# Kernel optimization log

Hardware: AMD Instinct MI355X
Metric: run time of the kernel (lower is better)

The kernel has to match this reference:

```python
import jax, jax.numpy as jnp
import numpy as np

D_MODEL = 1024
D_STATE = 16
DT_RANK = 64  # ceil(1024/16)
DT_MIN, DT_MAX = 1e-3, 1e-1


def setup_inputs() -> dict:
    key = jax.random.key(0)
    ks = jax.random.split(key, 6)
    x = jax.random.normal(ks[0], (2, 2048, D_MODEL), jnp.float32)
    A_log = jax.random.normal(ks[1], (D_MODEL, D_STATE), jnp.float32)
    D = jax.random.normal(ks[2], (D_MODEL,), jnp.float32)
    # nn.Linear default init ~ U(-1/sqrt(fan_in), 1/sqrt(fan_in)); normal*scale is fine for a baseline
    x_proj_w = jax.random.normal(ks[3], (DT_RANK + 2 * D_STATE, D_MODEL), jnp.float32) * (D_MODEL ** -0.5)
    dt_init_std = DT_RANK ** -0.5
    dt_proj_w = jax.random.uniform(ks[4], (D_MODEL, DT_RANK), jnp.float32, -dt_init_std, dt_init_std)
    dt = jnp.exp(jax.random.uniform(ks[5], (D_MODEL,), jnp.float32)
                 * (np.log(DT_MAX) - np.log(DT_MIN)) + np.log(DT_MIN))
    dt_proj_b = dt + jnp.log(-jnp.expm1(-dt))  # inverse-softplus init
    return {"x": x, "A_log": A_log, "D": D, "x_proj_w": x_proj_w,
            "dt_proj_w": dt_proj_w, "dt_proj_b": dt_proj_b}


def _s6(x, A_log, D, x_proj_w, dt_proj_w, dt_proj_b):
    A = -jnp.exp(A_log)                                    # (d, n)
    xp = jnp.einsum('bld,ed->ble', x, x_proj_w)            # (b, l, r+2n)
    d_rank = xp[..., :DT_RANK]
    Bm = xp[..., DT_RANK:DT_RANK + D_STATE]                # (b, l, n)
    Cm = xp[..., DT_RANK + D_STATE:]                       # (b, l, n)
    delta = jax.nn.softplus(jnp.einsum('blr,dr->bld', d_rank, dt_proj_w) + dt_proj_b)
    deltaA = jnp.exp(jnp.einsum('bld,dn->bldn', delta, A))          # (b, l, d, n)
    deltaB_u = jnp.einsum('bld,bln,bld->bldn', delta, Bm, x)        # (b, l, d, n)

    def step(h, inp):
        dA_t, dBu_t, C_t = inp          # (b,d,n), (b,d,n), (b,n)
        h = dA_t * h + dBu_t
        y = jnp.einsum('bdn,bn->bd', h, C_t)
        return h, y

    b, l, d = x.shape
    h0 = jnp.zeros((b, d, D_STATE), x.dtype)
    _, ys = jax.lax.scan(step, h0,
                         (deltaA.transpose(1, 0, 2, 3),
                          deltaB_u.transpose(1, 0, 2, 3),
                          Cm.transpose(1, 0, 2)))
    y = ys.transpose(1, 0, 2) + x * D                      # (b, l, d)
    return y


def reference(x, A_log, D, x_proj_w, dt_proj_w, dt_proj_b):
    return _s6(x, A_log, D, x_proj_w, dt_proj_w, dt_proj_b)
```

## Files before the change

### kernel.cpp

```cpp
#include <hip/hip_runtime.h>
#include <math.h>

#define Bb 2
#define Ll 2048
#define Dm 1024
#define Ns 16
#define Rr 64
#define Ee 96
#define XPS 8
#define BLK (Bb*Ll)
#define NTHR 256

__global__ void __launch_bounds__(NTHR)
k_xproj(const float* __restrict__ x, const float* __restrict__ xw,
        float* __restrict__ xp_part) {
    __shared__ float xsT[32 * 68];
    __shared__ float wT [32 * 100];
    int bx = blockIdx.x;
    int ks = bx & 7, mt = bx >> 3;
    int i0 = mt * 64;
    int tid = threadIdx.x;
    int tx = tid & 15, ty = tid >> 4;

    float acc[4][6];
#pragma unroll
    for (int ii = 0; ii < 4; ++ii)
#pragma unroll
        for (int jj = 0; jj < 6; ++jj) acc[ii][jj] = 0.f;

    for (int kc = 0; kc < 4; ++kc) {
        int k0 = ks * 128 + kc * 32;
        for (int t = tid; t < 512; t += NTHR) {
            int r = t >> 3, c = (t & 7) * 4;
            float4 v = *(const float4*)(x + (size_t)(i0 + r) * Dm + k0 + c);
            xsT[(c+0)*68 + r] = v.x; xsT[(c+1)*68 + r] = v.y;
            xsT[(c+2)*68 + r] = v.z; xsT[(c+3)*68 + r] = v.w;
        }
        for (int t = tid; t < 768; t += NTHR) {
            int r = t >> 3, c = (t & 7) * 4;
            float4 v = *(const float4*)(xw + (size_t)r * Dm + k0 + c);
            wT[(c+0)*100 + r] = v.x; wT[(c+1)*100 + r] = v.y;
            wT[(c+2)*100 + r] = v.z; wT[(c+3)*100 + r] = v.w;
        }
        __syncthreads();
#pragma unroll 8
        for (int k = 0; k < 32; ++k) {
            float xv[4], wv[6];
            *(float4*)xv     = *(const float4*)(xsT + k*68 + ty*4);
            *(float2*)(wv)   = *(const float2*)(wT + k*100 + tx*6);
            *(float2*)(wv+2) = *(const float2*)(wT + k*100 + tx*6 + 2);
            *(float2*)(wv+4) = *(const float2*)(wT + k*100 + tx*6 + 4);
#pragma unroll
            for (int ii = 0; ii < 4; ++ii)
#pragma unroll
                for (int jj = 0; jj < 6; ++jj)
                    acc[ii][jj] = fmaf(xv[ii], wv[jj], acc[ii][jj]);
        }
        __syncthreads();
    }
#pragma unroll
    for (int ii = 0; ii < 4; ++ii)
#pragma unroll
        for (int jj = 0; jj < 6; ++jj)
            xp_part[((size_t)ks * BLK + (i0 + ty*4 + ii)) * Ee + tx*6 + jj] = acc[ii][jj];
}

__global__ void __launch_bounds__(NTHR)
k_prep(const float* __restrict__ xp_part, float* __restrict__ xpR,
       float* __restrict__ xpBC) {
    int gid = blockIdx.x * NTHR + threadIdx.x;
    int r = gid / 24, c4 = gid % 24;
    float4 s = make_float4(0.f, 0.f, 0.f, 0.f);
#pragma unroll
    for (int i = 0; i < XPS; ++i) {
        float4 v = *(const float4*)(xp_part + ((size_t)i * BLK + r) * Ee + c4 * 4);
        s.x += v.x; s.y += v.y; s.z += v.z; s.w += v.w;
    }
    if (c4 < 16) *(float4*)(xpR  + (size_t)r * Rr + c4 * 4)        = s;
    else         *(float4*)(xpBC + (size_t)r * 32 + (c4 - 16) * 4) = s;
}

__global__ void __launch_bounds__(NTHR)
k_delta(const float* __restrict__ xpR, const float* __restrict__ dtw,
        const float* __restrict__ dtb, float* __restrict__ delta) {
    __shared__ float xsT[64 * 68];
    __shared__ float wT [64 * 68];
    int bx = blockIdx.x;
    int nt = bx & 15, mt = bx >> 4;
    int i0 = mt * 64, j0 = nt * 64;
    int tid = threadIdx.x, tx = tid & 15, ty = tid >> 4;

    for (int t = tid; t < 1024; t += NTHR) {
        int r = t >> 4, c = (t & 15) * 4;
        float4 v = *(const float4*)(xpR + (size_t)(i0 + r) * Rr + c);
        xsT[(c+0)*68 + r] = v.x; xsT[(c+1)*68 + r] = v.y;
        xsT[(c+2)*68 + r] = v.z; xsT[(c+3)*68 + r] = v.w;
        float4 w = *(const float4*)(dtw + (size_t)(j0 + r) * Rr + c);
        wT[(c+0)*68 + r] = w.x; wT[(c+1)*68 + r] = w.y;
        wT[(c+2)*68 + r] = w.z; wT[(c+3)*68 + r] = w.w;
    }
    __syncthreads();

    float acc[4][4];
#pragma unroll
    for (int ii = 0; ii < 4; ++ii)
#pragma unroll
        for (int jj = 0; jj < 4; ++jj) acc[ii][jj] = 0.f;
#pragma unroll 8
    for (int k = 0; k < 64; ++k) {
        float xv[4], wv[4];
        *(float4*)xv = *(const float4*)(xsT + k*68 + ty*4);
        *(float4*)wv = *(const float4*)(wT  + k*68 + tx*4);
#pragma unroll
        for (int ii = 0; ii < 4; ++ii)
#pragma unroll
            for (int jj = 0; jj < 4; ++jj)
                acc[ii][jj] = fmaf(xv[ii], wv[jj], acc[ii][jj]);
    }
    int d0 = j0 + tx * 4;
    float4 bias = *(const float4*)(dtb + d0);
#pragma unroll
    for (int ii = 0; ii < 4; ++ii) {
        int bl = i0 + ty*4 + ii;
        float z0 = acc[ii][0] + bias.x, z1 = acc[ii][1] + bias.y;
        float z2 = acc[ii][2] + bias.z, z3 = acc[ii][3] + bias.w;
        float4 o;
        o.x = fmaxf(z0, 0.f) + log1pf(__expf(-fabsf(z0)));
        o.y = fmaxf(z1, 0.f) + log1pf(__expf(-fabsf(z1)));
        o.z = fmaxf(z2, 0.f) + log1pf(__expf(-fabsf(z2)));
        o.w = fmaxf(z3, 0.f) + log1pf(__expf(-fabsf(z3)));
        *(float4*)(delta + (size_t)bl * Dm + d0) = o;
    }
}

__device__ inline void load_a(const float* __restrict__ A_log, int d, float* a) {
    const float4* Ap = (const float4*)(A_log + (size_t)d * Ns);
    float4 a0 = Ap[0], a1 = Ap[1], a2 = Ap[2], a3 = Ap[3];
    float tmp[Ns] = {a0.x,a0.y,a0.z,a0.w, a1.x,a1.y,a1.z,a1.w,
                     a2.x,a2.y,a2.z,a2.w, a3.x,a3.y,a3.z,a3.w};
#pragma unroll
    for (int n = 0; n < Ns; ++n) a[n] = -__expf(tmp[n]);
}

template<int CHv>
__global__ void __launch_bounds__(NTHR, 4)
k_scan_part(const float* __restrict__ delta, const float* __restrict__ x,
            const float* __restrict__ xpBC, const float* __restrict__ A_log,
            float* __restrict__ Ec, float* __restrict__ Sc) {
    constexpr int CLv = Ll / CHv;
    __shared__ float BCs[CLv * 32];
    int bx = blockIdx.x;
    int dblk = bx & 3, chunk = (bx >> 2) & (CHv - 1), b = bx >> 2 >> __builtin_ctz(CHv);
    int tid = threadIdx.x;
    int d = dblk * 256 + tid;
    int row0 = b * Ll + chunk * CLv;

    for (int t = tid; t < CLv * 8; t += NTHR) {
        int r = t >> 3, c = (t & 7) * 4;
        *(float4*)(BCs + r*32 + c) = *(const float4*)(xpBC + (size_t)(row0 + r) * 32 + c);
    }
    float a[Ns], h[Ns];
    load_a(A_log, d, a);
#pragma unroll
    for (int n = 0; n < Ns; ++n) h[n] = 0.f;
    float sd = 0.f;
    __syncthreads();

#pragma unroll 4
    for (int t = 0; t < CLv; ++t) {
        size_t row = (size_t)(row0 + t);
        float dl = delta[row * Dm + d];
        float xv = x[row * Dm + d];
        const float* bp = BCs + t*32;
        float4 B0 = *(const float4*)(bp + 0),  B1 = *(const float4*)(bp + 4);
        float4 B2 = *(const float4*)(bp + 8),  B3 = *(const float4*)(bp + 12);
        float Bv[Ns] = {B0.x,B0.y,B0.z,B0.w, B1.x,B1.y,B1.z,B1.w,
                        B2.x,B2.y,B2.z,B2.w, B3.x,B3.y,B3.z,B3.w};
        float dx = dl * xv;
        sd += dl;
#pragma unroll
        for (int n = 0; n < Ns; ++n)
            h[n] = fmaf(__expf(dl * a[n]), h[n], dx * Bv[n]);
    }
    size_t base = ((size_t)b * CHv + chunk) * Dm + d;
    float4* Ep = (float4*)(Ec + base * Ns);
    Ep[0] = make_float4(h[0],  h[1],  h[2],  h[3]);
    Ep[1] = make_float4(h[4],  h[5],  h[6],  h[7]);
    Ep[2] = make_float4(h[8],  h[9],  h[10], h[11]);
    Ep[3] = make_float4(h[12], h[13], h[14], h[15]);
    Sc[base] = sd;
}

template<int CHv>
__global__ void __launch_bounds__(NTHR)
k_combine(const float* __restrict__ Ec, const float* __restrict__ Sc,
          const float* __restrict__ A_log, float* __restrict__ Hin) {
    int gid = blockIdx.x * NTHR + threadIdx.x;
    int n = gid & (Ns - 1);
    int d = (gid >> 4) & (Dm - 1);
    int b = gid >> 14;
    float a = -__expf(A_log[d * Ns + n]);
    float h = 0.f;
    for (int c = 0; c < CHv; ++c) {
        size_t base = ((size_t)b * CHv + c) * Dm + d;
        Hin[base * Ns + n] = h;
        float P = __expf(a * Sc[base]);
        h = fmaf(P, h, Ec[base * Ns + n]);
    }
}

template<int CHv>
__global__ void __launch_bounds__(NTHR, 4)
k_scan_full(const float* __restrict__ delta, const float* __restrict__ x,
            const float* __restrict__ xpBC, const float* __restrict__ A_log,
            const float* __restrict__ Dp, const float* __restrict__ Hin,
            float* __restrict__ out) {
    constexpr int CLv = Ll / CHv;
    __shared__ float BCs[CLv * 32];
    int bx = blockIdx.x;
    int dblk = bx & 3, chunk = (bx >> 2) & (CHv - 1), b = bx >> 2 >> __builtin_ctz(CHv);
    int tid = threadIdx.x;
    int d = dblk * 256 + tid;
    int row0 = b * Ll + chunk * CLv;

    for (int t = tid; t < CLv * 8; t += NTHR) {
        int r = t >> 3, c = (t & 7) * 4;
        *(float4*)(BCs + r*32 + c) = *(const float4*)(xpBC + (size_t)(row0 + r) * 32 + c);
    }
    float a[Ns], h[Ns];
    load_a(A_log, d, a);
    size_t base = ((size_t)b * CHv + chunk) * Dm + d;
    {
        const float4* Hp = (const float4*)(Hin + base * Ns);
        float4 h0 = Hp[0], h1 = Hp[1], h2 = Hp[2], h3 = Hp[3];
        h[0]=h0.x; h[1]=h0.y; h[2]=h0.z; h[3]=h0.w;
        h[4]=h1.x; h[5]=h1.y; h[6]=h1.z; h[7]=h1.w;
        h[8]=h2.x; h[9]=h2.y; h[10]=h2.z; h[11]=h2.w;
        h[12]=h3.x; h[13]=h3.y; h[14]=h3.z; h[15]=h3.w;
    }
    float Dval = Dp[d];
    __syncthreads();

#pragma unroll 4
    for (int t = 0; t < CLv; ++t) {
        size_t row = (size_t)(row0 + t);
        float dl = delta[row * Dm + d];
        float xv = x[row * Dm + d];
        const float* bp = BCs + t*32;
        float4 B0 = *(const float4*)(bp + 0),  B1 = *(const float4*)(bp + 4);
        float4 B2 = *(const float4*)(bp + 8),  B3 = *(const float4*)(bp + 12);
        float4 C0 = *(const float4*)(bp + 16), C1 = *(const float4*)(bp + 20);
        float4 C2 = *(const float4*)(bp + 24), C3 = *(const float4*)(bp + 28);
        float Bv[Ns] = {B0.x,B0.y,B0.z,B0.w, B1.x,B1.y,B1.z,B1.w,
                        B2.x,B2.y,B2.z,B2.w, B3.x,B3.y,B3.z,B3.w};
        float Cv[Ns] = {C0.x,C0.y,C0.z,C0.w, C1.x,C1.y,C1.z,C1.w,
                        C2.x,C2.y,C2.z,C2.w, C3.x,C3.y,C3.z,C3.w};
        float dx = dl * xv;
        float y = 0.f;
#pragma unroll
        for (int n = 0; n < Ns; ++n) {
            h[n] = fmaf(__expf(dl * a[n]), h[n], dx * Bv[n]);
            y = fmaf(h[n], Cv[n], y);
        }
        out[row * Dm + d] = fmaf(xv, Dval, y);
    }
}

extern "C" void kernel_launch(void* const* d_in, const int* in_sizes, int n_in,
                              void* d_out, int out_size, void* d_ws, size_t ws_size,
                              hipStream_t stream) {
    const float* x     = (const float*)d_in[0];
    const float* A_log = (const float*)d_in[1];
    const float* Dp    = (const float*)d_in[2];
    const float* xw    = (const float*)d_in[3];
    const float* dtw   = (const float*)d_in[4];
    const float* dtb   = (const float*)d_in[5];
    float* out = (float*)d_out;
    float* ws  = (float*)d_ws;

    float* xpR     = ws;
    float* xpBC    = xpR  + 262144;
    float* delta   = xpBC + 131072;
    float* S3      = delta + 4194304;
    float* xp_part = S3;

    k_xproj<<<dim3(512),  dim3(NTHR), 0, stream>>>(x, xw, xp_part);
    k_prep <<<dim3(384),  dim3(NTHR), 0, stream>>>(xp_part, xpR, xpBC);
    k_delta<<<dim3(1024), dim3(NTHR), 0, stream>>>(xpR, dtw, dtb, delta);

    size_t need128 = (size_t)(262144 + 131072 + 4194304 + 8650752) * 4;
    if (ws_size >= need128) {
        constexpr int CHv = 128;
        float* Ec  = S3;
        float* Sc  = Ec + (size_t)Bb*CHv*Dm*Ns;
        float* Hin = Sc + (size_t)Bb*CHv*Dm;
        k_scan_part<CHv><<<dim3(Bb*CHv*4), dim3(NTHR), 0, stream>>>(delta, x, xpBC, A_log, Ec, Sc);
        k_combine  <CHv><<<dim3(128),      dim3(NTHR), 0, stream>>>(Ec, Sc, A_log, Hin);
        k_scan_full<CHv><<<dim3(Bb*CHv*4), dim3(NTHR), 0, stream>>>(delta, x, xpBC, A_log, Dp, Hin, out);
    } else {
        constexpr int CHv = 64;
        float* Ec  = S3;
        float* Sc  = Ec + (size_t)Bb*CHv*Dm*Ns;
        float* Hin = Sc + (size_t)Bb*CHv*Dm;
        k_scan_part<CHv><<<dim3(Bb*CHv*4), dim3(NTHR), 0, stream>>>(delta, x, xpBC, A_log, Ec, Sc);
        k_combine  <CHv><<<dim3(128),      dim3(NTHR), 0, stream>>>(Ec, Sc, A_log, Hin);
        k_scan_full<CHv><<<dim3(Bb*CHv*4), dim3(NTHR), 0, stream>>>(delta, x, xpBC, A_log, Dp, Hin, out);
    }
}
```

Baseline: 167.5 us.

## Fuse split-K reduction into delta GEMM and fix scan chunk count at 64

Removes the k_prep kernel: the delta GEMM now sums the split-K partials of the x-projection while loading its tile, and blocks with nt==0 also write the B/C columns. Scan kernels drop the workspace-size branch and template and always use 64 chunks of 32 steps, with a simplified shared-memory load and no occupancy hint. This saves a launch and an intermediate buffer round trip. In exchange, every delta block re-reads eight partial slices, and each scan thread runs a longer serial chain across fewer blocks.

Measured after the change: 179.1 us. 1.07x slower.

```diff
diff --git a/kernel.cpp b/kernel.cpp
--- a/kernel.cpp
+++ b/kernel.cpp
@@ -10,6 +10,8 @@
 #define XPS 8
 #define BLK (Bb*Ll)
 #define NTHR 256
+#define CH 64
+#define CL 32
 
 __global__ void __launch_bounds__(NTHR)
 k_xproj(const float* __restrict__ x, const float* __restrict__ xw,
@@ -66,23 +68,9 @@
 }
 
 __global__ void __launch_bounds__(NTHR)
-k_prep(const float* __restrict__ xp_part, float* __restrict__ xpR,
-       float* __restrict__ xpBC) {
-    int gid = blockIdx.x * NTHR + threadIdx.x;
-    int r = gid / 24, c4 = gid % 24;
-    float4 s = make_float4(0.f, 0.f, 0.f, 0.f);
-#pragma unroll
-    for (int i = 0; i < XPS; ++i) {
-        float4 v = *(const float4*)(xp_part + ((size_t)i * BLK + r) * Ee + c4 * 4);
-        s.x += v.x; s.y += v.y; s.z += v.z; s.w += v.w;
-    }
-    if (c4 < 16) *(float4*)(xpR  + (size_t)r * Rr + c4 * 4)        = s;
-    else         *(float4*)(xpBC + (size_t)r * 32 + (c4 - 16) * 4) = s;
-}
-
-__global__ void __launch_bounds__(NTHR)
-k_delta(const float* __restrict__ xpR, const float* __restrict__ dtw,
-        const float* __restrict__ dtb, float* __restrict__ delta) {
+k_delta(const float* __restrict__ xp_part, const float* __restrict__ dtw,
+        const float* __restrict__ dtb, float* __restrict__ delta,
+        float* __restrict__ xpBC) {
     __shared__ float xsT[64 * 68];
     __shared__ float wT [64 * 68];
     int bx = blockIdx.x;
@@ -92,12 +80,29 @@
 
     for (int t = tid; t < 1024; t += NTHR) {
         int r = t >> 4, c = (t & 15) * 4;
-        float4 v = *(const float4*)(xpR + (size_t)(i0 + r) * Rr + c);
-        xsT[(c+0)*68 + r] = v.x; xsT[(c+1)*68 + r] = v.y;
-        xsT[(c+2)*68 + r] = v.z; xsT[(c+3)*68 + r] = v.w;
+        float4 s = make_float4(0.f, 0.f, 0.f, 0.f);
+#pragma unroll
+        for (int i = 0; i < XPS; ++i) {
+            float4 v = *(const float4*)(xp_part + ((size_t)i * BLK + i0 + r) * Ee + c);
+            s.x += v.x; s.y += v.y; s.z += v.z; s.w += v.w;
+        }
+        xsT[(c+0)*68 + r] = s.x; xsT[(c+1)*68 + r] = s.y;
+        xsT[(c+2)*68 + r] = s.z; xsT[(c+3)*68 + r] = s.w;
         float4 w = *(const float4*)(dtw + (size_t)(j0 + r) * Rr + c);
         wT[(c+0)*68 + r] = w.x; wT[(c+1)*68 + r] = w.y;
         wT[(c+2)*68 + r] = w.z; wT[(c+3)*68 + r] = w.w;
+    }
+    if (nt == 0) {
+        for (int t = tid; t < 512; t += NTHR) {
+            int r = t >> 3, cc = (t & 7) * 4;
+            float4 s = make_float4(0.f, 0.f, 0.f, 0.f);
+#pragma unroll
+            for (int i = 0; i < XPS; ++i) {
+                float4 v = *(const float4*)(xp_part + ((size_t)i * BLK + i0 + r) * Ee + Rr + cc);
+                s.x += v.x; s.y += v.y; s.z += v.z; s.w += v.w;
+            }
+            *(float4*)(xpBC + (size_t)(i0 + r) * 32 + cc) = s;
+        }
     }
     __syncthreads();
 
@@ -142,21 +147,19 @@
     for (int n = 0; n < Ns; ++n) a[n] = -__expf(tmp[n]);
 }
 
-template<int CHv>
-__global__ void __launch_bounds__(NTHR, 4)
+__global__ void __launch_bounds__(NTHR)
 k_scan_part(const float* __restrict__ delta, const float* __restrict__ x,
             const float* __restrict__ xpBC, const float* __restrict__ A_log,
             float* __restrict__ Ec, float* __restrict__ Sc) {
-    constexpr int CLv = Ll / CHv;
-    __shared__ float BCs[CLv * 32];
-    int bx = blockIdx.x;
-    int dblk = bx & 3, chunk = (bx >> 2) & (CHv - 1), b = bx >> 2 >> __builtin_ctz(CHv);
+    __shared__ float BCs[CL * 32];
+    int bx = blockIdx.x;
+    int dblk = bx & 3, chunk = (bx >> 2) & (CH - 1), b = bx >> 8;
     int tid = threadIdx.x;
     int d = dblk * 256 + tid;
-    int row0 = b * Ll + chunk * CLv;
-
-    for (int t = tid; t < CLv * 8; t += NTHR) {
-        int r = t >> 3, c = (t & 7) * 4;
+    int row0 = b * Ll + chunk * CL;
+
+    {
+        int r = tid >> 3, c = (tid & 7) * 4;
         *(float4*)(BCs + r*32 + c) = *(const float4*)(xpBC + (size_t)(row0 + r) * 32 + c);
     }
     float a[Ns], h[Ns];
@@ -167,7 +170,7 @@
     __syncthreads();
 
 #pragma unroll 4
-    for (int t = 0; t < CLv; ++t) {
+    for (int t = 0; t < CL; ++t) {
         size_t row = (size_t)(row0 + t);
         float dl = delta[row * Dm + d];
         float xv = x[row * Dm + d];
@@ -182,7 +185,7 @@
         for (int n = 0; n < Ns; ++n)
             h[n] = fmaf(__expf(dl * a[n]), h[n], dx * Bv[n]);
     }
-    size_t base = ((size_t)b * CHv + chunk) * Dm + d;
+    size_t base = ((size_t)b * CH + chunk) * Dm + d;
     float4* Ep = (float4*)(Ec + base * Ns);
     Ep[0] = make_float4(h[0],  h[1],  h[2],  h[3]);
     Ep[1] = make_float4(h[4],  h[5],  h[6],  h[7]);
@@ -191,7 +194,6 @@
     Sc[base] = sd;
 }
 
-template<int CHv>
 __global__ void __launch_bounds__(NTHR)
 k_combine(const float* __restrict__ Ec, const float* __restrict__ Sc,
           const float* __restrict__ A_log, float* __restrict__ Hin) {
@@ -201,35 +203,34 @@
     int b = gid >> 14;
     float a = -__expf(A_log[d * Ns + n]);
     float h = 0.f;
-    for (int c = 0; c < CHv; ++c) {
-        size_t base = ((size_t)b * CHv + c) * Dm + d;
+#pragma unroll 4
+    for (int c = 0; c < CH; ++c) {
+        size_t base = ((size_t)b * CH + c) * Dm + d;
         Hin[base * Ns + n] = h;
         float P = __expf(a * Sc[base]);
         h = fmaf(P, h, Ec[base * Ns + n]);
     }
 }
 
-template<int CHv>
-__global__ void __launch_bounds__(NTHR, 4)
+__global__ void __launch_bounds__(NTHR)
 k_scan_full(const float* __restrict__ delta, const float* __restrict__ x,
             const float* __restrict__ xpBC, const float* __restrict__ A_log,
             const float* __restrict__ Dp, const float* __restrict__ Hin,
             float* __restrict__ out) {
-    constexpr int CLv = Ll / CHv;
-    __shared__ float BCs[CLv * 32];
-    int bx = blockIdx.x;
-    int dblk = bx & 3, chunk = (bx >> 2) & (CHv - 1), b = bx >> 2 >> __builtin_ctz(CHv);
+    __shared__ float BCs[CL * 32];
+    int bx = blockIdx.x;
+    int dblk = bx & 3, chunk = (bx >> 2) & (CH - 1), b = bx >> 8;
     int tid = threadIdx.x;
     int d = dblk * 256 + tid;
-    int row0 = b * Ll + chunk * CLv;
-
-    for (int t = tid; t < CLv * 8; t += NTHR) {
-        int r = t >> 3, c = (t & 7) * 4;
+    int row0 = b * Ll + chunk * CL;
+
+    {
+        int r = tid >> 3, c = (tid & 7) * 4;
         *(float4*)(BCs + r*32 + c) = *(const float4*)(xpBC + (size_t)(row0 + r) * 32 + c);
     }
     float a[Ns], h[Ns];
     load_a(A_log, d, a);
-    size_t base = ((size_t)b * CHv + chunk) * Dm + d;
+    size_t base = ((size_t)b * CH + chunk) * Dm + d;
     {
         const float4* Hp = (const float4*)(Hin + base * Ns);
         float4 h0 = Hp[0], h1 = Hp[1], h2 = Hp[2], h3 = Hp[3];
@@ -242,7 +243,7 @@
     __syncthreads();
 
 #pragma unroll 4
-    for (int t = 0; t < CLv; ++t) {
+    for (int t = 0; t < CL; ++t) {
         size_t row = (size_t)(row0 + t);
         float dl = delta[row * Dm + d];
         float xv = x[row * Dm + d];
@@ -278,32 +279,16 @@
     float* out = (float*)d_out;
     float* ws  = (float*)d_ws;
 
-    float* xpR     = ws;
-    float* xpBC    = xpR  + 262144;
-    float* delta   = xpBC + 131072;
-    float* S3      = delta + 4194304;
-    float* xp_part = S3;
-
-    k_xproj<<<dim3(512),  dim3(NTHR), 0, stream>>>(x, xw, xp_part);
-    k_prep <<<dim3(384),  dim3(NTHR), 0, stream>>>(xp_part, xpR, xpBC);
-    k_delta<<<dim3(1024), dim3(NTHR), 0, stream>>>(xpR, dtw, dtb, delta);
-
-    size_t need128 = (size_t)(262144 + 131072 + 4194304 + 8650752) * 4;
-    if (ws_size >= need128) {
-        constexpr int CHv = 128;
-        float* Ec  = S3;
-        float* Sc  = Ec + (size_t)Bb*CHv*Dm*Ns;
-        float* Hin = Sc + (size_t)Bb*CHv*Dm;
-        k_scan_part<CHv><<<dim3(Bb*CHv*4), dim3(NTHR), 0, stream>>>(delta, x, xpBC, A_log, Ec, Sc);
-        k_combine  <CHv><<<dim3(128),      dim3(NTHR), 0, stream>>>(Ec, Sc, A_log, Hin);
-        k_scan_full<CHv><<<dim3(Bb*CHv*4), dim3(NTHR), 0, stream>>>(delta, x, xpBC, A_log, Dp, Hin, out);
-    } else {
-        constexpr int CHv = 64;
-        float* Ec  = S3;
-        float* Sc  = Ec + (size_t)Bb*CHv*Dm*Ns;
-        float* Hin = Sc + (size_t)Bb*CHv*Dm;
-        k_scan_part<CHv><<<dim3(Bb*CHv*4), dim3(NTHR), 0, stream>>>(delta, x, xpBC, A_log, Ec, Sc);
-        k_combine  <CHv><<<dim3(128),      dim3(NTHR), 0, stream>>>(Ec, Sc, A_log, Hin);
-        k_scan_full<CHv><<<dim3(Bb*CHv*4), dim3(NTHR), 0, stream>>>(delta, x, xpBC, A_log, Dp, Hin, out);
-    }
-}
+    float* xpBC    = ws;
+    float* delta   = xpBC    + 131072;
+    float* xp_part = delta   + 4194304;
+    float* Ec      = xp_part + 3145728;
+    float* Sc      = Ec      + 2097152;
+    float* Hin     = Sc      + 131072;
+
+    k_xproj    <<<dim3(512),  dim3(NTHR), 0, stream>>>(x, xw, xp_part);
+    k_delta    <<<dim3(1024), dim3(NTHR), 0, stream>>>(xp_part, dtw, dtb, delta, xpBC);
+    k_scan_part<<<dim3(512),  dim3(NTHR), 0, stream>>>(delta, x, xpBC, A_log, Ec, Sc);
+    k_combine  <<<dim3(128),  dim3(NTHR), 0, stream>>>(Ec, Sc, A_log, Hin);
+    k_scan_full<<<dim3(512),  dim3(NTHR), 0, stream>>>(delta, x, xpBC, A_log, Dp, Hin, out);
+}
```
